# Optimization experiments

Measured on AMD Instinct MI355X. Metric: run time of the kernel, lower is better.

Reference implementation:

```python
import jax, jax.numpy as jnp
import numpy as np

D = 32
B = 4096
T = 256
HIDDEN = 64
DT = 0.005


def setup_inputs() -> dict:
    key = jax.random.key(0)
    ks = jax.random.split(key, 6)
    s1 = 1.0 / np.sqrt(D + 1)
    s2 = 1.0 / np.sqrt(HIDDEN)
    return {
        "z0": jax.random.normal(ks[0], (B, D), dtype=jnp.float32),
        "ts": jnp.arange(T, dtype=jnp.float32) * DT,
        "noise": jax.random.normal(ks[1], (T - 1, B, D), dtype=jnp.float32),
        "W1": jax.random.normal(ks[2], (D + 1, HIDDEN), dtype=jnp.float32) * s1,
        "b1": jnp.zeros((HIDDEN,), dtype=jnp.float32),
        "W2": jax.random.normal(ks[3], (HIDDEN, HIDDEN), dtype=jnp.float32) * s2,
        "b2": jnp.zeros((HIDDEN,), dtype=jnp.float32),
        "W3": jax.random.normal(ks[4], (HIDDEN, D), dtype=jnp.float32) * s2,
        "b3": jnp.zeros((D,), dtype=jnp.float32),
        "log_std": jnp.full((D,), -1.0, dtype=jnp.float32),
    }


def reference(z0, ts, noise, W1, b1, W2, b2, W3, b3, log_std):
    """Euler-Maruyama integration of the posterior SDE.

    dz = f_phi(t, z) dt + diag(exp(log_std)) dW,  dW = sqrt(dt) * noise.
    Returns ys of shape [T, B, D] with ys[0] = z0 (matches torchsde.sdeint).
    """
    std = jnp.exp(log_std)  # [D], constant diagonal diffusion
    dts = ts[1:] - ts[:-1]  # [T-1]

    def drift(t, y):
        # MLP on cat([t, y]): Linear -> tanh -> Linear -> tanh -> Linear
        tt = jnp.broadcast_to(t, (y.shape[0], 1)).astype(y.dtype)
        h = jnp.tanh(jnp.concatenate([tt, y], axis=-1) @ W1 + b1)
        h = jnp.tanh(h @ W2 + b2)
        return h @ W3 + b3  # [B, D]

    def step(y, xs):
        t, dt, dw = xs
        y_next = y + drift(t, y) * dt + std * jnp.sqrt(dt) * dw
        return y_next, y_next

    _, ys = jax.lax.scan(step, z0, (ts[:-1], dts, noise))
    return jnp.concatenate([z0[None], ys], axis=0)  # [T, B, D]
```

## Files before the change

kernel.cpp:

```cpp
#include <hip/hip_runtime.h>

#define NB 4096
#define NT 256

typedef __bf16 bf16x8 __attribute__((ext_vector_type(8)));
typedef __bf16 bf16x4 __attribute__((ext_vector_type(4)));
typedef float f32x4 __attribute__((ext_vector_type(4)));
typedef unsigned int u32;
typedef unsigned int u32x4 __attribute__((ext_vector_type(4)));
typedef unsigned long long u64;

static __device__ __forceinline__ f32x4 mfma16(bf16x8 a, bf16x8 b, f32x4 c) {
  return __builtin_amdgcn_mfma_f32_16x16x32_bf16(a, b, c, 0, 0, 0);
}

#define LDS_BARRIER() asm volatile("s_waitcnt lgkmcnt(0)\n\ts_barrier" ::: "memory")

static __device__ __forceinline__ float ftanh(float x) {
  float e = __builtin_amdgcn_exp2f(x * 2.885390082f);
  return __builtin_fmaf(-2.0f, __builtin_amdgcn_rcpf(e + 1.0f), 1.0f);
}

static __device__ __forceinline__ u64 pack4(const f32x4& v) {
  bf16x4 p;
  p[0] = (__bf16)ftanh(v[0]);
  p[1] = (__bf16)ftanh(v[1]);
  p[2] = (__bf16)ftanh(v[2]);
  p[3] = (__bf16)ftanh(v[3]);
  return __builtin_bit_cast(u64, p);
}

static __device__ __forceinline__ bf16x8 frag2(u64 lo, u64 hi) {
  u32x4 v;
  v[0] = (u32)lo; v[1] = (u32)(lo >> 32);
  v[2] = (u32)hi; v[3] = (u32)(hi >> 32);
  return __builtin_bit_cast(bf16x8, v);
}

__global__ __launch_bounds__(256) void sde_kernel(
    const float* __restrict__ z0, const float* __restrict__ ts,
    const float* __restrict__ noise, const float* __restrict__ W1,
    const float* __restrict__ b1, const float* __restrict__ W2,
    const float* __restrict__ b2, const float* __restrict__ W3,
    const float* __restrict__ b3, const float* __restrict__ log_std,
    float* __restrict__ out) {
  (void)ts;
  __shared__ u64 h1x[4][64];
  __shared__ u64 h2x[4][64];

  const int lane = threadIdx.x & 63;
  const int wv = threadIdx.x >> 6;
  const int c = lane & 15;
  const int g = lane >> 4;
  const int R = blockIdx.x * 16 + c;

  bf16x8 a1;
  bf16x8 a2[2];
  bf16x8 a3[2][2];
#pragma unroll
  for (int j = 0; j < 8; ++j) {
    int k = 16 * (j >> 2) + 4 * g + (j & 3);
    a1[j] = (__bf16)W1[(1 + k) * 64 + 16 * wv + c];
  }
#pragma unroll
  for (int kf = 0; kf < 2; ++kf)
#pragma unroll
    for (int j = 0; j < 8; ++j) {
      int k = 32 * kf + 16 * (j >> 2) + 4 * g + (j & 3);
      a2[kf][j] = (__bf16)W2[k * 64 + 16 * wv + c];
    }
#pragma unroll
  for (int ot = 0; ot < 2; ++ot)
#pragma unroll
    for (int kf = 0; kf < 2; ++kf)
#pragma unroll
      for (int j = 0; j < 8; ++j) {
        int k = 32 * kf + 16 * (j >> 2) + 4 * g + (j & 3);
        a3[ot][kf][j] = (__bf16)W3[k * 32 + 16 * ot + c];
      }

  f32x4 b1v, w1r0, b2v;
#pragma unroll
  for (int r = 0; r < 4; ++r) {
    int d = 16 * wv + 4 * g + r;
    b1v[r] = b1[d];
    w1r0[r] = W1[d];
    b2v[r] = b2[d];
  }
  f32x4 b3v[2], stdv[2];
#pragma unroll
  for (int ot = 0; ot < 2; ++ot)
#pragma unroll
    for (int r = 0; r < 4; ++r) {
      int d = 16 * ot + 4 * g + r;
      b3v[ot][r] = b3[d];
      stdv[ot][r] = expf(log_std[d]);
    }

  f32x4 y0v = *reinterpret_cast<const f32x4*>(z0 + (size_t)R * 32 + 4 * g);
  f32x4 y1v = *reinterpret_cast<const f32x4*>(z0 + (size_t)R * 32 + 16 + 4 * g);
  if (wv == 0)
    *reinterpret_cast<f32x4*>(out + (size_t)R * 32 + 4 * g) = y0v;
  if (wv == 1)
    *reinterpret_cast<f32x4*>(out + (size_t)R * 32 + 16 + 4 * g) = y1v;

  bf16x8 yb;
#pragma unroll
  for (int j = 0; j < 8; ++j)
    yb[j] = (__bf16)((j >> 2) ? y1v[j & 3] : y0v[j & 3]);

  const float* nzp0 = noise + ((size_t)0 * NB + R) * 32 + 4 * g;
  f32x4 nz0 = *reinterpret_cast<const f32x4*>(nzp0);
  f32x4 nz1 = *reinterpret_cast<const f32x4*>(nzp0 + 16);

  for (int t = 0; t < NT - 1; ++t) {
    int tn = (t < NT - 2) ? (t + 1) : (NT - 2);
    const float* nzp = noise + ((size_t)tn * NB + R) * 32 + 4 * g;
    f32x4 nzn0 = *reinterpret_cast<const f32x4*>(nzp);
    f32x4 nzn1 = *reinterpret_cast<const f32x4*>(nzp + 16);

    float tcur = (float)t * 0.005f;
    float dtv = (float)(t + 1) * 0.005f - tcur;
    float sdt = sqrtf(dtv);

    f32x4 d1 = mfma16(a1, yb, b1v + tcur * w1r0);
    h1x[wv][lane] = pack4(d1);
    LDS_BARRIER();

    u64 q0 = h1x[0][lane], q1 = h1x[1][lane];
    u64 q2 = h1x[2][lane], q3 = h1x[3][lane];
    bf16x8 hb0 = frag2(q0, q1);
    bf16x8 hb1 = frag2(q2, q3);
    f32x4 d2 = mfma16(a2[1], hb1, mfma16(a2[0], hb0, b2v));
    h2x[wv][lane] = pack4(d2);
    LDS_BARRIER();

    u64 p0 = h2x[0][lane], p1 = h2x[1][lane];
    u64 p2 = h2x[2][lane], p3 = h2x[3][lane];
    bf16x8 gb0 = frag2(p0, p1);
    bf16x8 gb1 = frag2(p2, p3);
    f32x4 d30 = mfma16(a3[0][1], gb1, mfma16(a3[0][0], gb0, b3v[0]));
    f32x4 d31 = mfma16(a3[1][1], gb1, mfma16(a3[1][0], gb0, b3v[1]));

    y0v = y0v + d30 * dtv + (stdv[0] * sdt) * nz0;
    y1v = y1v + d31 * dtv + (stdv[1] * sdt) * nz1;

    float* op = out + ((size_t)(t + 1) * NB + R) * 32 + 4 * g;
    if (wv == 0) *reinterpret_cast<f32x4*>(op) = y0v;
    if (wv == 1) *reinterpret_cast<f32x4*>(op + 16) = y1v;

#pragma unroll
    for (int j = 0; j < 8; ++j)
      yb[j] = (__bf16)((j >> 2) ? y1v[j & 3] : y0v[j & 3]);

    nz0 = nzn0;
    nz1 = nzn1;
  }
}

extern "C" void kernel_launch(void* const* d_in, const int* in_sizes, int n_in,
                              void* d_out, int out_size, void* d_ws, size_t ws_size,
                              hipStream_t stream) {
  (void)in_sizes; (void)n_in; (void)out_size; (void)d_ws; (void)ws_size;
  const float* z0   = (const float*)d_in[0];
  const float* ts   = (const float*)d_in[1];
  const float* nz   = (const float*)d_in[2];
  const float* W1   = (const float*)d_in[3];
  const float* b1   = (const float*)d_in[4];
  const float* W2   = (const float*)d_in[5];
  const float* b2   = (const float*)d_in[6];
  const float* W3   = (const float*)d_in[7];
  const float* b3   = (const float*)d_in[8];
  const float* lstd = (const float*)d_in[9];
  float* out = (float*)d_out;
  hipLaunchKernelGGL(sde_kernel, dim3(NB / 16), dim3(256), 0, stream,
                     z0, ts, nz, W1, b1, W2, b2, W3, b3, lstd, out);
}
```

Before: 185.4 us.

## Process two 16-row batch tiles per block and use rational tanh approximation

```diff
diff --git a/kernel.cpp b/kernel.cpp
--- a/kernel.cpp
+++ b/kernel.cpp
@@ -16,17 +16,38 @@
 
 #define LDS_BARRIER() asm volatile("s_waitcnt lgkmcnt(0)\n\ts_barrier" ::: "memory")
 
-static __device__ __forceinline__ float ftanh(float x) {
-  float e = __builtin_amdgcn_exp2f(x * 2.885390082f);
-  return __builtin_fmaf(-2.0f, __builtin_amdgcn_rcpf(e + 1.0f), 1.0f);
-}
-
-static __device__ __forceinline__ u64 pack4(const f32x4& v) {
+static __device__ __forceinline__ f32x4 tanh4(f32x4 x) {
+  const float A1 = 4.89352455891786e-03f, A3 = 6.37261928875436e-04f,
+              A5 = 1.48572235717979e-05f, A7 = 5.12229709037114e-08f,
+              A9 = -8.60467152213735e-11f, A11 = 2.00018790482477e-13f,
+              A13 = -2.76076847742355e-16f;
+  const float B0 = 4.89352518554385e-03f, B2 = 2.26843463243900e-03f,
+              B4 = 1.18534705686654e-04f, B6 = 1.19825839466702e-06f;
+  f32x4 r;
+#pragma unroll
+  for (int i = 0; i < 4; ++i) {
+    float xi = fminf(fmaxf(x[i], -7.90531110763549805f), 7.90531110763549805f);
+    float u = xi * xi;
+    float p = __builtin_fmaf(u, A13, A11);
+    p = __builtin_fmaf(u, p, A9);
+    p = __builtin_fmaf(u, p, A7);
+    p = __builtin_fmaf(u, p, A5);
+    p = __builtin_fmaf(u, p, A3);
+    p = __builtin_fmaf(u, p, A1);
+    p = xi * p;
+    float q = __builtin_fmaf(u, B6, B4);
+    q = __builtin_fmaf(u, q, B2);
+    q = __builtin_fmaf(u, q, B0);
+    r[i] = p * __builtin_amdgcn_rcpf(q);
+  }
+  return r;
+}
+
+static __device__ __forceinline__ u64 pack4t(f32x4 v) {
+  f32x4 t = tanh4(v);
   bf16x4 p;
-  p[0] = (__bf16)ftanh(v[0]);
-  p[1] = (__bf16)ftanh(v[1]);
-  p[2] = (__bf16)ftanh(v[2]);
-  p[3] = (__bf16)ftanh(v[3]);
+  p[0] = (__bf16)t[0]; p[1] = (__bf16)t[1];
+  p[2] = (__bf16)t[2]; p[3] = (__bf16)t[3];
   return __builtin_bit_cast(u64, p);
 }
 
@@ -45,14 +66,16 @@
     const float* __restrict__ b3, const float* __restrict__ log_std,
     float* __restrict__ out) {
   (void)ts;
-  __shared__ u64 h1x[4][64];
-  __shared__ u64 h2x[4][64];
+  __shared__ u64 h1x[2][4][64];
+  __shared__ u64 h2x[2][4][64];
 
   const int lane = threadIdx.x & 63;
   const int wv = threadIdx.x >> 6;
   const int c = lane & 15;
   const int g = lane >> 4;
-  const int R = blockIdx.x * 16 + c;
+  int R[2];
+  R[0] = blockIdx.x * 32 + c;
+  R[1] = R[0] + 16;
 
   bf16x8 a1;
   bf16x8 a2[2];
@@ -97,64 +120,85 @@
       stdv[ot][r] = expf(log_std[d]);
     }
 
-  f32x4 y0v = *reinterpret_cast<const f32x4*>(z0 + (size_t)R * 32 + 4 * g);
-  f32x4 y1v = *reinterpret_cast<const f32x4*>(z0 + (size_t)R * 32 + 16 + 4 * g);
-  if (wv == 0)
-    *reinterpret_cast<f32x4*>(out + (size_t)R * 32 + 4 * g) = y0v;
-  if (wv == 1)
-    *reinterpret_cast<f32x4*>(out + (size_t)R * 32 + 16 + 4 * g) = y1v;
-
-  bf16x8 yb;
-#pragma unroll
-  for (int j = 0; j < 8; ++j)
-    yb[j] = (__bf16)((j >> 2) ? y1v[j & 3] : y0v[j & 3]);
-
-  const float* nzp0 = noise + ((size_t)0 * NB + R) * 32 + 4 * g;
-  f32x4 nz0 = *reinterpret_cast<const f32x4*>(nzp0);
-  f32x4 nz1 = *reinterpret_cast<const f32x4*>(nzp0 + 16);
+  f32x4 y0v[2], y1v[2];
+  bf16x8 yb[2];
+#pragma unroll
+  for (int tl = 0; tl < 2; ++tl) {
+    y0v[tl] = *reinterpret_cast<const f32x4*>(z0 + (size_t)R[tl] * 32 + 4 * g);
+    y1v[tl] = *reinterpret_cast<const f32x4*>(z0 + (size_t)R[tl] * 32 + 16 + 4 * g);
+    if (wv == 0)
+      *reinterpret_cast<f32x4*>(out + (size_t)R[tl] * 32 + 4 * g) = y0v[tl];
+    if (wv == 1)
+      *reinterpret_cast<f32x4*>(out + (size_t)R[tl] * 32 + 16 + 4 * g) = y1v[tl];
+#pragma unroll
+    for (int j = 0; j < 8; ++j)
+      yb[tl][j] = (__bf16)((j >> 2) ? y1v[tl][j & 3] : y0v[tl][j & 3]);
+  }
+
+  f32x4 nz0[2], nz1[2];
+#pragma unroll
+  for (int tl = 0; tl < 2; ++tl) {
+    const float* nzp = noise + ((size_t)0 * NB + R[tl]) * 32 + 4 * g;
+    nz0[tl] = *reinterpret_cast<const f32x4*>(nzp);
+    nz1[tl] = *reinterpret_cast<const f32x4*>(nzp + 16);
+  }
 
   for (int t = 0; t < NT - 1; ++t) {
     int tn = (t < NT - 2) ? (t + 1) : (NT - 2);
-    const float* nzp = noise + ((size_t)tn * NB + R) * 32 + 4 * g;
-    f32x4 nzn0 = *reinterpret_cast<const f32x4*>(nzp);
-    f32x4 nzn1 = *reinterpret_cast<const f32x4*>(nzp + 16);
+    f32x4 nzn0[2], nzn1[2];
+#pragma unroll
+    for (int tl = 0; tl < 2; ++tl) {
+      const float* nzp = noise + ((size_t)tn * NB + R[tl]) * 32 + 4 * g;
+      nzn0[tl] = *reinterpret_cast<const f32x4*>(nzp);
+      nzn1[tl] = *reinterpret_cast<const f32x4*>(nzp + 16);
+    }
 
     float tcur = (float)t * 0.005f;
     float dtv = (float)(t + 1) * 0.005f - tcur;
     float sdt = sqrtf(dtv);
-
-    f32x4 d1 = mfma16(a1, yb, b1v + tcur * w1r0);
-    h1x[wv][lane] = pack4(d1);
+    f32x4 cinit = b1v + tcur * w1r0;
+
+#pragma unroll
+    for (int tl = 0; tl < 2; ++tl) {
+      f32x4 d1 = mfma16(a1, yb[tl], cinit);
+      h1x[tl][wv][lane] = pack4t(d1);
+    }
     LDS_BARRIER();
 
-    u64 q0 = h1x[0][lane], q1 = h1x[1][lane];
-    u64 q2 = h1x[2][lane], q3 = h1x[3][lane];
-    bf16x8 hb0 = frag2(q0, q1);
-    bf16x8 hb1 = frag2(q2, q3);
-    f32x4 d2 = mfma16(a2[1], hb1, mfma16(a2[0], hb0, b2v));
-    h2x[wv][lane] = pack4(d2);
+#pragma unroll
+    for (int tl = 0; tl < 2; ++tl) {
+      u64 q0 = h1x[tl][0][lane], q1 = h1x[tl][1][lane];
+      u64 q2 = h1x[tl][2][lane], q3 = h1x[tl][3][lane];
+      bf16x8 hb0 = frag2(q0, q1);
+      bf16x8 hb1 = frag2(q2, q3);
+      f32x4 d2 = mfma16(a2[1], hb1, mfma16(a2[0], hb0, b2v));
+      h2x[tl][wv][lane] = pack4t(d2);
+    }
     LDS_BARRIER();
 
-    u64 p0 = h2x[0][lane], p1 = h2x[1][lane];
-    u64 p2 = h2x[2][lane], p3 = h2x[3][lane];
-    bf16x8 gb0 = frag2(p0, p1);
-    bf16x8 gb1 = frag2(p2, p3);
-    f32x4 d30 = mfma16(a3[0][1], gb1, mfma16(a3[0][0], gb0, b3v[0]));
-    f32x4 d31 = mfma16(a3[1][1], gb1, mfma16(a3[1][0], gb0, b3v[1]));
-
-    y0v = y0v + d30 * dtv + (stdv[0] * sdt) * nz0;
-    y1v = y1v + d31 * dtv + (stdv[1] * sdt) * nz1;
-
-    float* op = out + ((size_t)(t + 1) * NB + R) * 32 + 4 * g;
-    if (wv == 0) *reinterpret_cast<f32x4*>(op) = y0v;
-    if (wv == 1) *reinterpret_cast<f32x4*>(op + 16) = y1v;
-
-#pragma unroll
-    for (int j = 0; j < 8; ++j)
-      yb[j] = (__bf16)((j >> 2) ? y1v[j & 3] : y0v[j & 3]);
-
-    nz0 = nzn0;
-    nz1 = nzn1;
+#pragma unroll
+    for (int tl = 0; tl < 2; ++tl) {
+      u64 p0 = h2x[tl][0][lane], p1 = h2x[tl][1][lane];
+      u64 p2 = h2x[tl][2][lane], p3 = h2x[tl][3][lane];
+      bf16x8 gb0 = frag2(p0, p1);
+      bf16x8 gb1 = frag2(p2, p3);
+      f32x4 d30 = mfma16(a3[0][1], gb1, mfma16(a3[0][0], gb0, b3v[0]));
+      f32x4 d31 = mfma16(a3[1][1], gb1, mfma16(a3[1][0], gb0, b3v[1]));
+
+      y0v[tl] = y0v[tl] + d30 * dtv + (stdv[0] * sdt) * nz0[tl];
+      y1v[tl] = y1v[tl] + d31 * dtv + (stdv[1] * sdt) * nz1[tl];
+
+      float* op = out + ((size_t)(t + 1) * NB + R[tl]) * 32 + 4 * g;
+      if (wv == 0) *reinterpret_cast<f32x4*>(op) = y0v[tl];
+      if (wv == 1) *reinterpret_cast<f32x4*>(op + 16) = y1v[tl];
+
+#pragma unroll
+      for (int j = 0; j < 8; ++j)
+        yb[tl][j] = (__bf16)((j >> 2) ? y1v[tl][j & 3] : y0v[tl][j & 3]);
+
+      nz0[tl] = nzn0[tl];
+      nz1[tl] = nzn1[tl];
+    }
   }
 }
 
@@ -173,6 +217,6 @@
   const float* b3   = (const float*)d_in[8];
   const float* lstd = (const float*)d_in[9];
   float* out = (float*)d_out;
-  hipLaunchKernelGGL(sde_kernel, dim3(NB / 16), dim3(256), 0, stream,
+  hipLaunchKernelGGL(sde_kernel, dim3(NB / 32), dim3(256), 0, stream,
                      z0, ts, nz, W1, b1, W2, b2, W3, b3, lstd, out);
 }
```

New measurement: 307.8 us. 1.66x slower.

## Fold tanh affine into weights, split MFMA chains, defer output stores

Applied to the files above, without the earlier changes.

```diff
diff --git a/kernel.cpp b/kernel.cpp
--- a/kernel.cpp
+++ b/kernel.cpp
@@ -16,17 +16,17 @@
 
 #define LDS_BARRIER() asm volatile("s_waitcnt lgkmcnt(0)\n\ts_barrier" ::: "memory")
 
-static __device__ __forceinline__ float ftanh(float x) {
+static __device__ __forceinline__ float sigc(float x) {
   float e = __builtin_amdgcn_exp2f(x * 2.885390082f);
-  return __builtin_fmaf(-2.0f, __builtin_amdgcn_rcpf(e + 1.0f), 1.0f);
+  return __builtin_amdgcn_rcpf(e + 1.0f);
 }
 
-static __device__ __forceinline__ u64 pack4(const f32x4& v) {
+static __device__ __forceinline__ u64 pack4s(f32x4 v) {
   bf16x4 p;
-  p[0] = (__bf16)ftanh(v[0]);
-  p[1] = (__bf16)ftanh(v[1]);
-  p[2] = (__bf16)ftanh(v[2]);
-  p[3] = (__bf16)ftanh(v[3]);
+  p[0] = (__bf16)sigc(v[0]);
+  p[1] = (__bf16)sigc(v[1]);
+  p[2] = (__bf16)sigc(v[2]);
+  p[3] = (__bf16)sigc(v[3]);
   return __builtin_bit_cast(u64, p);
 }
 
@@ -67,7 +67,7 @@
 #pragma unroll
     for (int j = 0; j < 8; ++j) {
       int k = 32 * kf + 16 * (j >> 2) + 4 * g + (j & 3);
-      a2[kf][j] = (__bf16)W2[k * 64 + 16 * wv + c];
+      a2[kf][j] = (__bf16)(-2.0f * W2[k * 64 + 16 * wv + c]);
     }
 #pragma unroll
   for (int ot = 0; ot < 2; ++ot)
@@ -76,26 +76,36 @@
 #pragma unroll
       for (int j = 0; j < 8; ++j) {
         int k = 32 * kf + 16 * (j >> 2) + 4 * g + (j & 3);
-        a3[ot][kf][j] = (__bf16)W3[k * 32 + 16 * ot + c];
+        a3[ot][kf][j] = (__bf16)(-2.0f * W3[k * 32 + 16 * ot + c]);
       }
 
-  f32x4 b1v, w1r0, b2v;
+  f32x4 b1v, w1r0;
 #pragma unroll
   for (int r = 0; r < 4; ++r) {
     int d = 16 * wv + 4 * g + r;
     b1v[r] = b1[d];
     w1r0[r] = W1[d];
-    b2v[r] = b2[d];
   }
-  f32x4 b3v[2], stdv[2];
+  f32x4 b2s;
+#pragma unroll
+  for (int r = 0; r < 4; ++r) {
+    int d = 16 * wv + 4 * g + r;
+    float s = b2[d];
+    for (int j = 0; j < 64; ++j) s += W2[j * 64 + d];
+    b2s[r] = s;
+  }
+  f32x4 b3s[2], stdv[2];
 #pragma unroll
   for (int ot = 0; ot < 2; ++ot)
 #pragma unroll
     for (int r = 0; r < 4; ++r) {
       int d = 16 * ot + 4 * g + r;
-      b3v[ot][r] = b3[d];
+      float s = b3[d];
+      for (int j = 0; j < 64; ++j) s += W3[j * 32 + d];
+      b3s[ot][r] = s;
       stdv[ot][r] = expf(log_std[d]);
     }
+  const f32x4 zero4 = {0.0f, 0.0f, 0.0f, 0.0f};
 
   f32x4 y0v = *reinterpret_cast<const f32x4*>(z0 + (size_t)R * 32 + 4 * g);
   f32x4 y1v = *reinterpret_cast<const f32x4*>(z0 + (size_t)R * 32 + 16 + 4 * g);
@@ -109,53 +119,63 @@
   for (int j = 0; j < 8; ++j)
     yb[j] = (__bf16)((j >> 2) ? y1v[j & 3] : y0v[j & 3]);
 
+  f32x4 pend0 = y0v, pend1 = y1v;
+  float* pendp = out + (size_t)R * 32 + 4 * g;
+
   const float* nzp0 = noise + ((size_t)0 * NB + R) * 32 + 4 * g;
   f32x4 nz0 = *reinterpret_cast<const f32x4*>(nzp0);
   f32x4 nz1 = *reinterpret_cast<const f32x4*>(nzp0 + 16);
 
   for (int t = 0; t < NT - 1; ++t) {
+    float tcur = (float)t * 0.005f;
+
+    f32x4 d1 = mfma16(a1, yb, b1v + tcur * w1r0);
+    h1x[wv][lane] = pack4s(d1);
+    LDS_BARRIER();
+
+    u64 q0 = h1x[0][lane], q1 = h1x[1][lane];
+    u64 q2 = h1x[2][lane], q3 = h1x[3][lane];
+    if (wv == 0) *reinterpret_cast<f32x4*>(pendp) = pend0;
+    if (wv == 1) *reinterpret_cast<f32x4*>(pendp + 16) = pend1;
     int tn = (t < NT - 2) ? (t + 1) : (NT - 2);
     const float* nzp = noise + ((size_t)tn * NB + R) * 32 + 4 * g;
     f32x4 nzn0 = *reinterpret_cast<const f32x4*>(nzp);
     f32x4 nzn1 = *reinterpret_cast<const f32x4*>(nzp + 16);
-
-    float tcur = (float)t * 0.005f;
     float dtv = (float)(t + 1) * 0.005f - tcur;
     float sdt = sqrtf(dtv);
-
-    f32x4 d1 = mfma16(a1, yb, b1v + tcur * w1r0);
-    h1x[wv][lane] = pack4(d1);
-    LDS_BARRIER();
-
-    u64 q0 = h1x[0][lane], q1 = h1x[1][lane];
-    u64 q2 = h1x[2][lane], q3 = h1x[3][lane];
     bf16x8 hb0 = frag2(q0, q1);
     bf16x8 hb1 = frag2(q2, q3);
-    f32x4 d2 = mfma16(a2[1], hb1, mfma16(a2[0], hb0, b2v));
-    h2x[wv][lane] = pack4(d2);
+    f32x4 accA = mfma16(a2[0], hb0, b2s);
+    f32x4 accB = mfma16(a2[1], hb1, zero4);
+    h2x[wv][lane] = pack4s(accA + accB);
     LDS_BARRIER();
 
     u64 p0 = h2x[0][lane], p1 = h2x[1][lane];
     u64 p2 = h2x[2][lane], p3 = h2x[3][lane];
+    f32x4 s0 = stdv[0] * sdt;
+    f32x4 s1 = stdv[1] * sdt;
     bf16x8 gb0 = frag2(p0, p1);
     bf16x8 gb1 = frag2(p2, p3);
-    f32x4 d30 = mfma16(a3[0][1], gb1, mfma16(a3[0][0], gb0, b3v[0]));
-    f32x4 d31 = mfma16(a3[1][1], gb1, mfma16(a3[1][0], gb0, b3v[1]));
+    f32x4 dA0 = mfma16(a3[0][0], gb0, b3s[0]);
+    f32x4 dB0 = mfma16(a3[0][1], gb1, zero4);
+    f32x4 dA1 = mfma16(a3[1][0], gb0, b3s[1]);
+    f32x4 dB1 = mfma16(a3[1][1], gb1, zero4);
+    f32x4 d30 = dA0 + dB0;
+    f32x4 d31 = dA1 + dB1;
 
-    y0v = y0v + d30 * dtv + (stdv[0] * sdt) * nz0;
-    y1v = y1v + d31 * dtv + (stdv[1] * sdt) * nz1;
-
-    float* op = out + ((size_t)(t + 1) * NB + R) * 32 + 4 * g;
-    if (wv == 0) *reinterpret_cast<f32x4*>(op) = y0v;
-    if (wv == 1) *reinterpret_cast<f32x4*>(op + 16) = y1v;
-
+    y0v = y0v + d30 * dtv + s0 * nz0;
+    y1v = y1v + d31 * dtv + s1 * nz1;
 #pragma unroll
     for (int j = 0; j < 8; ++j)
       yb[j] = (__bf16)((j >> 2) ? y1v[j & 3] : y0v[j & 3]);
-
+    pend0 = y0v;
+    pend1 = y1v;
+    pendp = out + ((size_t)(t + 1) * NB + R) * 32 + 4 * g;
     nz0 = nzn0;
     nz1 = nzn1;
   }
+  if (wv == 0) *reinterpret_cast<f32x4*>(pendp) = pend0;
+  if (wv == 1) *reinterpret_cast<f32x4*>(pendp + 16) = pend1;
 }
 
 extern "C" void kernel_launch(void* const* d_in, const int* in_sizes, int n_in,
```

Result: no change. 185.5 us (+0.1%).
